# Performance work log

Hardware: AMD Instinct MI355X
Metric: run time of the kernel (lower is better)

Reference implementation:

```python
import jax, jax.numpy as jnp
import numpy as np

B, NUM, NVAR = 2048, 100, 11
NUM_OBS, NC = 10, 3
T_FIN = 10.0
RHO_OBS = 1.0; RHO_INEQ = 1.0; RHO_LANE = 1.0; RHO_PROJ = 1.0
W_SMOOTH = 20.0; W_VDES = 2.0; W_YDES = 1.0
A_EGO = 3.0; B_EGO = 1.5; MARGIN = 0.2
V_MIN = 0.001; V_MAX = 18.0; A_MAX = 6.0
MAXITER = 5
H = 256

def _basis():
    s = np.linspace(0.0, 1.0, NUM)
    j = np.arange(NVAR)
    P = s[:, None] ** j[None, :]
    Pd = np.zeros((NUM, NVAR)); Pdd = np.zeros((NUM, NVAR))
    Pd[:, 1:] = j[1:][None, :] * s[:, None] ** (j[1:] - 1)[None, :]
    Pdd[:, 2:] = (j[2:] * (j[2:] - 1))[None, :] * s[:, None] ** (j[2:] - 2)[None, :]
    return (jnp.asarray(P, jnp.float32), jnp.asarray(Pd / T_FIN, jnp.float32),
            jnp.asarray(Pdd / (T_FIN ** 2), jnp.float32))

P, PDOT, PDDOT = _basis()
A_EQ_X = jnp.stack([P[0], PDOT[0], PDDOT[0], P[-1]])   # [4, NVAR]
A_EQ_Y = jnp.stack([P[0], PDOT[0], PDDOT[0]])          # [3, NVAR]
PTP = P.T @ P

def _kkt_inv(Q, A):
    m = A.shape[0]
    K = jnp.concatenate([jnp.concatenate([Q, A.T], axis=1),
                         jnp.concatenate([A, jnp.zeros((m, m), jnp.float32)], axis=1)], axis=0)
    return jnp.linalg.inv(K)

# ADMM cost: rho_proj*I + smoothness + rho_obs*A_obs^T A_obs + rho_ineq*(Pdot^T Pdot + Pddot^T Pddot)
Q_COMMON = (RHO_PROJ + W_SMOOTH) * jnp.eye(NVAR, dtype=jnp.float32) \
    + RHO_OBS * NUM_OBS * NC * PTP \
    + RHO_INEQ * (PDOT.T @ PDOT + PDDOT.T @ PDDOT)
KKT_X = _kkt_inv(Q_COMMON, A_EQ_X)
KKT_Y = _kkt_inv(Q_COMMON + 2.0 * RHO_LANE * PTP, A_EQ_Y)   # A_lane = [P; -P]
# x_init QP (smoothness + v_des / y_des tracking)
Q_IX = W_SMOOTH * jnp.eye(NVAR, dtype=jnp.float32) + W_VDES * (PDOT.T @ PDOT)
KKT_IX = _kkt_inv(Q_IX, A_EQ_X)
KKT_IY = _kkt_inv(Q_IX + W_YDES * PTP, A_EQ_Y)


def _forward(init_state_ego, goal_des, closest_obs, psi_obs, dim_x_obs, dim_y_obs,
             y_ub, y_lb, gru_W_ih, gru_W_hh, gru_b, gru_h0,
             mlp_W1, mlp_b1, mlp_W2, mlp_b2):
    b = init_state_ego.shape[0]
    x0, y0, vx0, vy0, ax0, ay0 = (init_state_ego[:, i] for i in range(6))
    b_eq_x = jnp.stack([x0, vx0, ax0, goal_des[:, 0]], axis=1)   # [B,4]
    b_eq_y = jnp.stack([y0, vy0, ay0], axis=1)                    # [B,3]

    # ---- obstacle circle trajectories (static obstacles, vx=vy=0) ----
    xo = closest_obs[:, :NUM_OBS]; yo = closest_obs[:, NUM_OBS:2 * NUM_OBS]   # [B,O]
    r = jnp.stack([jnp.zeros_like(dim_x_obs),
                   (dim_x_obs - dim_y_obs) / 2,
                   -(dim_x_obs - dim_y_obs) / 2], axis=2)                      # [B,O,3]
    x_circ = xo[:, :, None] + r * jnp.cos(psi_obs)[:, :, None]                # [B,O,3]
    y_circ = yo[:, :, None] + r * jnp.sin(psi_obs)[:, :, None]
    shape4 = (b, NUM_OBS, NC, NUM)
    x_obs_f = jnp.broadcast_to(x_circ[..., None], shape4).reshape(b, -1)      # [B,O*C*T]
    y_obs_f = jnp.broadcast_to(y_circ[..., None], shape4).reshape(b, -1)
    rad = dim_y_obs / 2
    a_obs = jnp.broadcast_to((A_EGO + rad + MARGIN)[:, :, None, None], shape4).reshape(b, -1)
    b_obs = jnp.broadcast_to((B_EGO + rad + MARGIN)[:, :, None, None], shape4).reshape(b, -1)

    # ---- GRU context over obstacles -> learned lambda init ----
    feats = jnp.stack([xo, yo, dim_x_obs, dim_y_obs, psi_obs], axis=2)        # [B,O,5]
    def gru_step(h, x):
        gx = x @ gru_W_ih + gru_b
        gh = h @ gru_W_hh
        z = jax.nn.sigmoid(gx[:, :H] + gh[:, :H])
        rg = jax.nn.sigmoid(gx[:, H:2 * H] + gh[:, H:2 * H])
        n = jnp.tanh(gx[:, 2 * H:] + rg * gh[:, 2 * H:])
        return (1.0 - z) * n + z * h, None
    hT, _ = jax.lax.scan(gru_step, jnp.broadcast_to(gru_h0, (b, H)), jnp.swapaxes(feats, 0, 1))
    lam = jax.nn.relu(hT @ mlp_W1 + mlp_b1) @ mlp_W2 + mlp_b2                 # [B,2*NVAR]
    lam_x, lam_y = lam[:, :NVAR], lam[:, NVAR:]

    # ---- x_init: equality-constrained smoothness/tracking QP ----
    v_des = jnp.sqrt(vx0 ** 2 + vy0 ** 2)
    lin_ix = W_VDES * v_des[:, None] * jnp.sum(PDOT, axis=0)[None, :]
    lin_iy = W_YDES * goal_des[:, 1:2] * jnp.sum(P, axis=0)[None, :]
    c_x0 = (jnp.concatenate([lin_ix, b_eq_x], 1) @ KKT_IX.T)[:, :NVAR]
    c_y0 = (jnp.concatenate([lin_iy, b_eq_y], 1) @ KKT_IY.T)[:, :NVAR]

    b_lane = jnp.concatenate([y_ub[:, None] * jnp.ones((1, NUM), jnp.float32),
                              -y_lb[:, None] * jnp.ones((1, NUM), jnp.float32)], axis=1)  # [B,2T]

    def AobsT(v):   # A_obs^T v, v: [B, O*C*T] -> [B, NVAR]
        return v.reshape(b, NUM_OBS * NC, NUM).sum(axis=1) @ P

    def step(carry, _):
        c_x, c_y, lx, ly = carry
        x = c_x @ P.T; xd = c_x @ PDOT.T; xdd = c_x @ PDDOT.T
        y = c_y @ P.T; yd = c_y @ PDOT.T; ydd = c_y @ PDDOT.T
        wc = jnp.tile(x, (1, NUM_OBS * NC)) - x_obs_f
        ws = jnp.tile(y, (1, NUM_OBS * NC)) - y_obs_f
        alpha_o = jnp.arctan2(ws * a_obs, wc * b_obs)
        ca, sa = jnp.cos(alpha_o), jnp.sin(alpha_o)
        c1 = RHO_OBS * (a_obs ** 2 * ca ** 2 + b_obs ** 2 * sa ** 2)
        c2 = RHO_OBS * (a_obs * wc * ca + b_obs * ws * sa)
        d_o = jnp.maximum(1.0, c2 / c1)
        alpha_v = jnp.clip(jnp.arctan2(yd, xd), -0.41, 0.41)
        cv, sv = jnp.cos(alpha_v), jnp.sin(alpha_v)
        d_v = jnp.clip(xd * cv + yd * sv, V_MIN, V_MAX)
        alpha_a = jnp.arctan2(ydd + 1e-4, xdd + 1e-4)
        caa, saa = jnp.cos(alpha_a), jnp.sin(alpha_a)
        d_a = jnp.clip(xdd * caa + ydd * saa, 0.0, A_MAX)
        # targets
        b_ox = x_obs_f + a_obs * d_o * ca; b_oy = y_obs_f + b_obs * d_o * sa
        b_vx = d_v * cv; b_vy = d_v * sv
        b_ax = d_a * caa; b_ay = d_a * saa
        b_lane_aug = jnp.minimum(jnp.concatenate([y, -y], 1), b_lane)  # slack-augmented
        top_x = lx + RHO_PROJ * c_x0 + RHO_OBS * AobsT(b_ox) + RHO_INEQ * (b_vx @ PDOT + b_ax @ PDDOT)
        top_y = ly + RHO_PROJ * c_y0 + RHO_OBS * AobsT(b_oy) + RHO_INEQ * (b_vy @ PDOT + b_ay @ PDDOT) \
            + RHO_LANE * ((b_lane_aug[:, :NUM] - b_lane_aug[:, NUM:]) @ P)
        c_xn = (jnp.concatenate([top_x, b_eq_x], 1) @ KKT_X.T)[:, :NVAR]
        c_yn = (jnp.concatenate([top_y, b_eq_y], 1) @ KKT_Y.T)[:, :NVAR]
        # residuals / Lagrange multiplier updates
        xn = c_xn @ P.T; yn = c_yn @ P.T
        res_ox = jnp.tile(xn, (1, NUM_OBS * NC)) - b_ox
        res_oy = jnp.tile(yn, (1, NUM_OBS * NC)) - b_oy
        lxn = lx - RHO_OBS * AobsT(res_ox) \
            - RHO_INEQ * ((c_xn @ PDOT.T - b_vx) @ PDOT + (c_xn @ PDDOT.T - b_ax) @ PDDOT)
        res_lane = jnp.concatenate([yn, -yn], 1) - b_lane_aug
        lyn = ly - RHO_OBS * AobsT(res_oy) \
            - RHO_INEQ * ((c_yn @ PDOT.T - b_vy) @ PDOT + (c_yn @ PDDOT.T - b_ay) @ PDDOT) \
            - RHO_LANE * ((res_lane[:, :NUM] - res_lane[:, NUM:]) @ P)
        return (c_xn, c_yn, lxn, lyn), None

    (c_x, c_y, lam_x, lam_y), _ = jax.lax.scan(step, (c_x0, c_y0, lam_x, lam_y),
                                               None, length=MAXITER)
    return jnp.concatenate([c_x, c_y], axis=1)   # [B, 2*NVAR]


def setup_inputs() -> dict:
    key = jax.random.key(0)
    ks = jax.random.split(key, 12)
    d = {
        'init_state_ego': jax.random.normal(ks[0], (B, 6), jnp.float32),
        'goal_des': jax.random.normal(ks[1], (B, 2), jnp.float32),
        'closest_obs': jax.random.normal(ks[2], (B, 2 * NUM_OBS), jnp.float32),
        'psi_obs': jax.random.normal(ks[3], (B, NUM_OBS), jnp.float32),
        'dim_x_obs': jax.random.uniform(ks[4], (B, NUM_OBS), jnp.float32),
        'dim_y_obs': jax.random.uniform(ks[5], (B, NUM_OBS), jnp.float32),
        'y_ub': jnp.ones((B,), jnp.float32),
        'y_lb': jnp.zeros((B,), jnp.float32),
        'gru_W_ih': jax.random.normal(ks[6], (5, 3 * H), jnp.float32) / np.sqrt(5.0),
        'gru_W_hh': jax.random.normal(ks[7], (H, 3 * H), jnp.float32) / np.sqrt(float(H)),
        'gru_b': jnp.zeros((3 * H,), jnp.float32),
        'gru_h0': jax.random.normal(ks[8], (H,), jnp.float32) * 0.1,
        'mlp_W1': jax.random.normal(ks[9], (H, 512), jnp.float32) / np.sqrt(float(H)),
        'mlp_b1': jnp.zeros((512,), jnp.float32),
        'mlp_W2': jax.random.normal(ks[10], (512, 2 * NVAR), jnp.float32) / np.sqrt(512.0),
        'mlp_b2': jnp.zeros((2 * NVAR,), jnp.float32),
    }
    return d


def reference(init_state_ego, goal_des, closest_obs, psi_obs, dim_x_obs, dim_y_obs,
              y_ub, y_lb, gru_W_ih, gru_W_hh, gru_b, gru_h0,
              mlp_W1, mlp_b1, mlp_W2, mlp_b2):
    return _forward(init_state_ego, goal_des, closest_obs, psi_obs, dim_x_obs, dim_y_obs,
                    y_ub, y_lb, gru_W_ih, gru_W_hh, gru_b, gru_h0,
                    mlp_W1, mlp_b1, mlp_W2, mlp_b2)
```

## Files before the change

kernel.cpp:

```cpp
#include <hip/hip_runtime.h>
#include <math.h>

typedef short bf16x8 __attribute__((ext_vector_type(8)));
typedef float f32x4 __attribute__((ext_vector_type(4)));

__device__ __forceinline__ unsigned short f2bf(float x) {
  union { float f; unsigned u; } v; v.f = x;
  unsigned r = v.u + 0x7FFFu + ((v.u >> 16) & 1u);
  return (unsigned short)(r >> 16);
}
__device__ __forceinline__ float bf2f(unsigned short h) {
  union { unsigned u; float f; } v; v.u = ((unsigned)h) << 16; return v.f;
}

#define WS_WAUG  0u
#define WS_W1T   442368u
#define WS_HAUGA 704512u
#define WS_HAUGB 1884160u
#define WS_HF32  3063808u
#define WS_ACTS  3063808u
#define WS_LAM   5160960u
#define WS_KKT   5341184u
#define WS_GX    5344000u
#define WS_GY    5344704u
#define WS_MX    5345408u
#define WS_MY    5346112u
#define WS_SUMS  5346816u

__global__ __launch_bounds__(256) void prep(
    const float* __restrict__ Whh, const float* __restrict__ Wih,
    const float* __restrict__ gb, const float* __restrict__ W1,
    const float* __restrict__ h0,
    const float* __restrict__ obs, const float* __restrict__ dimx,
    const float* __restrict__ dimy, const float* __restrict__ psi,
    unsigned short* __restrict__ Waug, unsigned short* __restrict__ W1T,
    unsigned short* __restrict__ HaugA, unsigned short* __restrict__ HaugB,
    float* __restrict__ kkt_out, float* __restrict__ Gx_out,
    float* __restrict__ Gy_out, float* __restrict__ Mx_out,
    float* __restrict__ My_out, float* __restrict__ sums_out)
{
  __shared__ double S[21];
  __shared__ double aug[15][32];
  __shared__ double fbuf[15];
  __shared__ double Md[11][11];
  if (blockIdx.x < 4) {
    const int mat = blockIdx.x;
    const int n = (mat == 0 || mat == 2) ? 15 : 14;
    const int twoN = 2 * n;
    if (threadIdx.x == 0) {
      for (int m = 0; m < 21; ++m) S[m] = 0.0;
      for (int s = 0; s < 100; ++s) {
        double t = s * (1.0 / 99.0);
        double p = 1.0;
        for (int m = 0; m < 21; ++m) { S[m] += p; p *= t; }
      }
    }
    __syncthreads();
    for (int idx = threadIdx.x; idx < n * twoN; idx += 256) {
      int r = idx / twoN, c = idx % twoN;
      double v;
      if (c >= n) v = (c - n == r) ? 1.0 : 0.0;
      else if (r < 11 && c < 11) {
        double ptp = S[r + c];
        double pdp = (r >= 1 && c >= 1) ? ((double)(r * c) / 100.0) * S[r + c - 2] : 0.0;
        double pddp = (r >= 2 && c >= 2) ? ((double)(r*(r-1)) * (double)(c*(c-1)) / 10000.0) * S[r + c - 4] : 0.0;
        double dg = (r == c) ? 1.0 : 0.0;
        if (mat == 0)      v = 21.0*dg + 30.0*ptp + pdp + pddp;
        else if (mat == 1) v = 21.0*dg + 32.0*ptp + pdp + pddp;
        else if (mat == 2) v = 20.0*dg + 2.0*pdp;
        else               v = 20.0*dg + 2.0*pdp + ptp;
      } else if (r >= 11 && c >= 11) v = 0.0;
      else {
        int ar = (r >= 11) ? (r - 11) : (c - 11);
        int ac = (r >= 11) ? c : r;
        v = (ar == 0) ? ((ac == 0) ? 1.0 : 0.0)
          : (ar == 1) ? ((ac == 1) ? 0.1 : 0.0)
          : (ar == 2) ? ((ac == 2) ? 0.02 : 0.0)
          : 1.0;
      }
      aug[r][c] = v;
    }
    __syncthreads();
    for (int p = 0; p < n; ++p) {
      double pv = aug[p][p];
      __syncthreads();
      double inv = 1.0 / pv;
      for (int c = threadIdx.x; c < twoN; c += 256) aug[p][c] *= inv;
      __syncthreads();
      if (threadIdx.x < n) fbuf[threadIdx.x] = aug[threadIdx.x][p];
      __syncthreads();
      for (int idx = threadIdx.x; idx < n * twoN; idx += 256) {
        int r = idx / twoN, c = idx % twoN;
        if (r != p) aug[r][c] -= fbuf[r] * aug[p][c];
      }
      __syncthreads();
    }
    for (int idx = threadIdx.x; idx < 11 * n; idx += 256) {
      int r = idx / n, c = idx % n;
      kkt_out[mat * 176 + r * 16 + c] = (float)aug[r][n + c];
    }
    if (mat < 2) {
      if (threadIdx.x < 121) {
        int j = threadIdx.x / 11, i = threadIdx.x % 11;
        double m = 30.0 * S[j + i];
        if (j >= 1 && i >= 1) m += ((double)(j * i) / 100.0) * S[j + i - 2];
        if (j >= 2 && i >= 2) m += ((double)(j*(j-1)) * (double)(i*(i-1)) / 10000.0) * S[j + i - 4];
        if (mat == 1) m += 2.0 * S[j + i];
        Md[j][i] = m;
      }
      __syncthreads();
      if (threadIdx.x < 121) {
        int j = threadIdx.x / 11, i = threadIdx.x % 11;
        double g = (j == i) ? 1.0 : 0.0;
        for (int k = 0; k < 11; ++k) g -= Md[j][k] * aug[k][n + i];
        if (mat == 0) { Gx_out[j * 16 + i] = (float)g; Mx_out[j * 16 + i] = (float)Md[j][i]; }
        else          { Gy_out[j * 16 + i] = (float)g; My_out[j * 16 + i] = (float)Md[j][i]; }
      }
    }
    if (mat == 0 && threadIdx.x < 11) {
      int j = threadIdx.x;
      sums_out[j] = (float)S[j];
      sums_out[11 + j] = (j >= 1) ? (float)((double)j / 10.0 * S[j - 1]) : 0.f;
    }
    return;
  }
  int idx = (blockIdx.x - 4) * 256 + threadIdx.x;
  if (idx < 221184) {
    int col = idx / 288, k = idx - col * 288;
    float v;
    if (k < 256)       v = Whh[k * 768 + col];
    else if (k < 261)  v = Wih[(k - 256) * 768 + col];
    else if (k == 261) v = gb[col];
    else               v = 0.f;
    Waug[idx] = f2bf(v);
  } else if (idx < 352256) {
    int j = idx - 221184;
    int col = j >> 8, k = j & 255;
    W1T[j] = f2bf(W1[k * 512 + col]);
  } else if (idx < 942080) {
    int j = idx - 352256;
    int row = j / 288, k = j - row * 288;
    float v;
    if (k < 256)       v = h0[k];
    else if (k == 256) v = obs[row * 20 + 0];
    else if (k == 257) v = obs[row * 20 + 10];
    else if (k == 258) v = dimx[row * 10 + 0];
    else if (k == 259) v = dimy[row * 10 + 0];
    else if (k == 260) v = psi[row * 10 + 0];
    else if (k == 261) v = 1.0f;
    else               v = 0.f;
    HaugA[row * 288 + k] = f2bf(v);
  } else if (idx < 995328) {
    int j = idx - 942080;
    int row = j / 26, k = 262 + (j - row * 26);
    HaugB[row * 288 + k] = 0;
  }
}

#define MFMA __builtin_amdgcn_mfma_f32_16x16x32_bf16
__global__ __launch_bounds__(256) void gru_step(
    const unsigned short* __restrict__ Waug,
    const unsigned short* __restrict__ HaugC, unsigned short* __restrict__ HaugN,
    float* __restrict__ Hf32, const float* __restrict__ h0,
    const float* __restrict__ obs, const float* __restrict__ dimx,
    const float* __restrict__ dimy, const float* __restrict__ psi,
    int s)
{
  const int tid = threadIdx.x;
  const int m0 = blockIdx.x * 32;
  const int c0 = blockIdx.y * 32;
  const int lane = tid & 63, w = tid >> 6;
  const int l15 = lane & 15, g4 = lane >> 4;
  const int mi = w >> 1, cg = w & 1;

  const unsigned short* Arow = HaugC + (size_t)(m0 + mi * 16 + l15) * 288 + g4 * 8;
  const unsigned short* Bcol = Waug + (size_t)(c0 + cg * 16 + l15) * 288 + g4 * 8;

  f32x4 accz = {0.f,0.f,0.f,0.f}, accr = {0.f,0.f,0.f,0.f};
  f32x4 anh = {0.f,0.f,0.f,0.f}, anx = {0.f,0.f,0.f,0.f};

  #pragma unroll
  for (int kc = 0; kc < 9; ++kc) {
    bf16x8 a  = *(const bf16x8*)(Arow + kc * 32);
    bf16x8 bz = *(const bf16x8*)(Bcol + kc * 32);
    bf16x8 br = *(const bf16x8*)(Bcol + 256 * 288 + kc * 32);
    bf16x8 bn = *(const bf16x8*)(Bcol + 512 * 288 + kc * 32);
    accz = MFMA(a, bz, accz, 0, 0, 0);
    accr = MFMA(a, br, accr, 0, 0, 0);
    if (kc < 8) anh = MFMA(a, bn, anh, 0, 0, 0);
    else        anx = MFMA(a, bn, anx, 0, 0, 0);
  }

  const int colh = c0 + cg * 16 + l15;
  float h0c = (s == 0) ? h0[colh] : 0.f;
  #pragma unroll
  for (int rg = 0; rg < 4; ++rg) {
    int row = m0 + mi * 16 + g4 * 4 + rg;
    float hold = (s == 0) ? h0c : Hf32[(size_t)row * 256 + colh];
    float z = 1.f / (1.f + __expf(-accz[rg]));
    float rr = 1.f / (1.f + __expf(-accr[rg]));
    float nn = tanhf(anx[rg] + rr * anh[rg]);
    float hnew = (1.f - z) * nn + z * hold;
    Hf32[(size_t)row * 256 + colh] = hnew;
    HaugN[(size_t)row * 288 + colh] = f2bf(hnew);
  }
  if (blockIdx.y == 0 && s < 9 && tid < 192) {
    int row = m0 + tid / 6, e = tid - (tid / 6) * 6;
    int s1 = s + 1;
    float v = (e == 0) ? obs[row * 20 + s1] : (e == 1) ? obs[row * 20 + 10 + s1]
            : (e == 2) ? dimx[row * 10 + s1] : (e == 3) ? dimy[row * 10 + s1]
            : (e == 4) ? psi[row * 10 + s1] : 1.0f;
    HaugN[(size_t)row * 288 + 256 + e] = f2bf(v);
  }
}

__global__ __launch_bounds__(256) void mlp1(
    const unsigned short* __restrict__ Haug, const unsigned short* __restrict__ W1T,
    const float* __restrict__ b1, unsigned short* __restrict__ acts)
{
  __shared__ __align__(16) unsigned short As[8192];
  const int tid = threadIdx.x;
  const int m0 = blockIdx.x * 32, c0 = blockIdx.y * 128;
  const int lane = tid & 63, w = tid >> 6, l15 = lane & 15, g4 = lane >> 4;

  #pragma unroll
  for (int r = 0; r < 4; ++r) {
    int j = tid + 256 * r;
    int tile = j >> 6, q = j & 63, ci = q >> 2, ks = q & 3;
    int mi = tile >> 3, kc = tile & 7;
    const unsigned short* src = Haug + (size_t)(m0 + mi * 16 + ci) * 288 + kc * 32 + ks * 8;
    *(int4*)&As[tile * 512 + q * 8] = *(const int4*)src;
  }
  __syncthreads();

  const int foff = (l15 * 4 + g4) * 8;
  f32x4 acc[2][2];
  #pragma unroll
  for (int a = 0; a < 2; ++a)
    #pragma unroll
    for (int b = 0; b < 2; ++b) acc[a][b] = (f32x4){0.f,0.f,0.f,0.f};

  #pragma unroll
  for (int kc = 0; kc < 8; ++kc) {
    bf16x8 a0 = *(const bf16x8*)&As[(0 * 8 + kc) * 512 + foff];
    bf16x8 a1 = *(const bf16x8*)&As[(1 * 8 + kc) * 512 + foff];
    int kk = kc * 32 + g4 * 8;
    #pragma unroll
    for (int nt = 0; nt < 2; ++nt) {
      int col = c0 + w * 32 + nt * 16 + l15;
      bf16x8 b = *(const bf16x8*)&W1T[(size_t)col * 256 + kk];
      acc[0][nt] = MFMA(a0, b, acc[0][nt], 0, 0, 0);
      acc[1][nt] = MFMA(a1, b, acc[1][nt], 0, 0, 0);
    }
  }
  #pragma unroll
  for (int mi = 0; mi < 2; ++mi)
    #pragma unroll
    for (int nt = 0; nt < 2; ++nt) {
      int col = c0 + w * 32 + nt * 16 + l15;
      float bb = b1[col];
      #pragma unroll
      for (int rg = 0; rg < 4; ++rg) {
        int row = m0 + mi * 16 + g4 * 4 + rg;
        float v = fmaxf(acc[mi][nt][rg] + bb, 0.f);
        acts[(size_t)row * 512 + col] = f2bf(v);
      }
    }
}

__global__ __launch_bounds__(256) void mlp2(
    const unsigned short* __restrict__ acts, const float* __restrict__ W2,
    const float* __restrict__ b2, float* __restrict__ lam)
{
  __shared__ unsigned short Ablk[8 * 520];
  __shared__ float W2s[512 * 22];
  const int tid = threadIdx.x;
  const int m0 = blockIdx.x * 8;
  for (int i = tid; i < 4096; i += 256) {
    int r = i >> 9, k = i & 511;
    Ablk[r * 520 + k] = acts[(size_t)(m0 + r) * 512 + k];
  }
  for (int i = tid; i < 11264; i += 256) W2s[i] = W2[i];
  __syncthreads();
  if (tid < 176) {
    int row = tid / 22, col = tid - (tid / 22) * 22;
    float s = b2[col];
    const unsigned short* ap = &Ablk[row * 520];
    for (int k = 0; k < 512; ++k) s += bf2f(ap[k]) * W2s[k * 22 + col];
    lam[(size_t)(m0 + row) * 22 + col] = s;
  }
}

__global__ __launch_bounds__(128) void solver(
    const float* __restrict__ ise, const float* __restrict__ goal,
    const float* __restrict__ obs, const float* __restrict__ psi,
    const float* __restrict__ dimx, const float* __restrict__ dimy,
    const float* __restrict__ yub, const float* __restrict__ ylb,
    const float* __restrict__ lam, const float* __restrict__ kkt,
    const float* __restrict__ Gxm, const float* __restrict__ Gym,
    const float* __restrict__ Mxm, const float* __restrict__ Mym,
    const float* __restrict__ sums, float* __restrict__ out)
{
  __shared__ __align__(16) float Pt[3][11][108];
  __shared__ __align__(16) float red[7][108];
  __shared__ float redout[7][11];
  __shared__ float cx[11], cy[11], lx[11], ly[11], cx0[11], cy0[11];
  __shared__ float kxB[11], kyB[11], hx[11], hy[11];
  __shared__ float rhsx[15], rhsy[14];
  __shared__ float xc[30], yc[30], sa_[10], sb_[10], sab[10], sab2[10];

  const int b = blockIdx.x;
  const int tid = threadIdx.x;

  if (tid < 100) {
    float t = tid * (1.0f / 99.0f);
    float tjm2 = 0.f, tjm1 = 0.f, tj = 1.f;
    #pragma unroll
    for (int j = 0; j < 11; ++j) {
      Pt[0][j][tid] = tj;
      Pt[1][j][tid] = 0.1f * (float)j * tjm1;
      Pt[2][j][tid] = 0.01f * (float)(j * (j - 1)) * tjm2;
      tjm2 = tjm1; tjm1 = tj; tj *= t;
    }
  }
  if (tid < 10) {
    int o = tid;
    float xo = obs[b * 20 + o], yo = obs[b * 20 + 10 + o];
    float dx = dimx[b * 10 + o], dy = dimy[b * 10 + o], ps = psi[b * 10 + o];
    float sp, cp;
    __sincosf(ps, &sp, &cp);
    float r1 = 0.5f * (dx - dy);
    xc[o * 3] = xo; xc[o * 3 + 1] = xo + r1 * cp; xc[o * 3 + 2] = xo - r1 * cp;
    yc[o * 3] = yo; yc[o * 3 + 1] = yo + r1 * sp; yc[o * 3 + 2] = yo - r1 * sp;
    float rad = 0.5f * dy;
    float av = 3.2f + rad, bv = 1.7f + rad;
    sa_[o] = av; sb_[o] = bv; sab[o] = av * bv; sab2[o] = av * bv * av * bv;
  }
  if (tid < 11) { lx[tid] = lam[b * 22 + tid]; ly[tid] = lam[b * 22 + 11 + tid]; }
  const float vx0 = ise[b * 6 + 2], vy0 = ise[b * 6 + 3];
  if (tid == 0) {
    float x0 = ise[b * 6 + 0], y0 = ise[b * 6 + 1];
    float ax0 = ise[b * 6 + 4], ay0 = ise[b * 6 + 5];
    rhsx[11] = x0; rhsx[12] = vx0; rhsx[13] = ax0; rhsx[14] = goal[b * 2 + 0];
    rhsy[11] = y0; rhsy[12] = vy0; rhsy[13] = ay0;
  }
  {
    float vdes = sqrtf(vx0 * vx0 + vy0 * vy0);
    float gy = goal[b * 2 + 1];
    if (tid < 11) { rhsx[tid] = 2.f * vdes * sums[11 + tid]; rhsy[tid] = gy * sums[tid]; }
  }
  const float yU = yub[b], yL = ylb[b];
  __syncthreads();
  if (tid < 11) {
    const float* K = kkt + 2 * 176 + tid * 16;
    float s = 0.f;
    #pragma unroll
    for (int j = 0; j < 15; ++j) s += K[j] * rhsx[j];
    cx0[tid] = s; cx[tid] = s;
    const float* Kx = kkt + tid * 16;
    float kb = 0.f;
    #pragma unroll
    for (int c = 0; c < 4; ++c) kb += Kx[11 + c] * rhsx[11 + c];
    kxB[tid] = kb;
  } else if (tid >= 16 && tid < 27) {
    int i = tid - 16;
    const float* K = kkt + 3 * 176 + i * 16;
    float s = 0.f;
    #pragma unroll
    for (int j = 0; j < 14; ++j) s += K[j] * rhsy[j];
    cy0[i] = s; cy[i] = s;
    const float* Ky = kkt + 176 + i * 16;
    float kb = 0.f;
    #pragma unroll
    for (int c = 0; c < 3; ++c) kb += Ky[11 + c] * rhsy[11 + c];
    kyB[i] = kb;
  }
  __syncthreads();
  if (tid < 11) {
    float s = cx0[tid];
    #pragma unroll
    for (int i = 0; i < 11; ++i) s += Mxm[tid * 16 + i] * kxB[i];
    hx[tid] = s;
  } else if (tid >= 16 && tid < 27) {
    int j = tid - 16;
    float s = cy0[j];
    #pragma unroll
    for (int i = 0; i < 11; ++i) s += Mym[j * 16 + i] * kyB[i];
    hy[j] = s;
  }
  __syncthreads();

  for (int it = 0; it < 5; ++it) {
    if (tid < 100) {
      float t = tid * (1.0f / 99.0f);
      float x = 0, y = 0, xd = 0, yd = 0, xdd = 0, ydd = 0;
      {
        float tjm2 = 0, tjm1 = 0, tj = 1;
        #pragma unroll
        for (int j = 0; j < 11; ++j) {
          float cj = cx[j], dj = cy[j];
          x += cj * tj; y += dj * tj;
          float pd = 0.1f * (float)j * tjm1;
          xd += cj * pd; yd += dj * pd;
          float pdd = 0.01f * (float)(j * (j - 1)) * tjm2;
          xdd += cj * pdd; ydd += dj * pdd;
          tjm2 = tjm1; tjm1 = tj; tj *= t;
        }
      }
      float Sbx = 0.f, Sby = 0.f;
      for (int oi = 0; oi < 10; ++oi) {
        float A = sa_[oi], B = sb_[oi], AB = sab[oi], AB2 = sab2[oi];
        #pragma unroll
        for (int cc = 0; cc < 3; ++cc) {
          int o = oi * 3 + cc;
          float xcc = xc[o], ycc = yc[o];
          float wc = x - xcc, wsv = y - ycc;
          float p = wsv * A, q = wc * B;
          float h2 = p * p + q * q;
          float rin = rsqrtf(h2 + 1e-20f);
          float sc = AB * rin;
          bool outside = h2 >= AB2;
          Sbx += outside ? x : fmaf(wc, sc, xcc);
          Sby += outside ? y : fmaf(wsv, sc, ycc);
        }
      }
      bool clipv = (xd <= 0.f) || (fabsf(yd) > xd * 0.43463135f);
      float cv, sv;
      if (clipv) { cv = 0.91712081f; sv = copysignf(0.39860934f, yd); }
      else { float ri = rsqrtf(fmaxf(xd * xd + yd * yd, 1e-24f)); cv = xd * ri; sv = yd * ri; }
      float dv = fminf(fmaxf(xd * cv + yd * sv, 0.001f), 18.f);
      float qa = xdd + 1e-4f, pa = ydd + 1e-4f;
      float ria = rsqrtf(pa * pa + qa * qa + 1e-30f);
      float caa = qa * ria, saa = pa * ria;
      float da = fminf(fmaxf(xdd * caa + ydd * saa, 0.f), 6.f);
      red[0][tid] = Sbx; red[1][tid] = Sby;
      red[2][tid] = dv * cv; red[3][tid] = dv * sv;
      red[4][tid] = da * caa; red[5][tid] = da * saa;
      red[6][tid] = fminf(y, yU) - fminf(-y, -yL);
    }
    __syncthreads();
    if (tid < 77) {
      int a = tid / 11, j = tid - a * 11;
      int wt = (a < 2) ? 0 : (a < 4) ? 1 : (a < 6) ? 2 : 0;
      const float4* rp = (const float4*)(&red[a][0]);
      const float4* wp = (const float4*)(&Pt[wt][j][0]);
      float s = 0.f;
      #pragma unroll
      for (int k = 0; k < 25; ++k) {
        float4 rv = rp[k], wv = wp[k];
        s += rv.x * wv.x + rv.y * wv.y + rv.z * wv.z + rv.w * wv.w;
      }
      redout[a][j] = s;
    }
    __syncthreads();
    if (tid < 11) rhsx[tid] = lx[tid] + cx0[tid] + redout[0][tid] + redout[2][tid] + redout[4][tid];
    else if (tid >= 16 && tid < 27) {
      int j = tid - 16;
      rhsy[j] = ly[j] + cy0[j] + redout[1][j] + redout[3][j] + redout[5][j] + redout[6][j];
    }
    __syncthreads();
    if (tid < 11) {
      const float* K = kkt + tid * 16;
      const float* G = Gxm + tid * 16;
      float sc = kxB[tid], sl = -hx[tid];
      #pragma unroll
      for (int i = 0; i < 11; ++i) {
        float r = rhsx[i];
        sc += K[i] * r;
        sl += G[i] * r;
      }
      cx[tid] = sc; lx[tid] = sl;
    } else if (tid >= 16 && tid < 27) {
      int j = tid - 16;
      const float* K = kkt + 176 + j * 16;
      const float* G = Gym + j * 16;
      float sc = kyB[j], sl = -hy[j];
      #pragma unroll
      for (int i = 0; i < 11; ++i) {
        float r = rhsy[i];
        sc += K[i] * r;
        sl += G[i] * r;
      }
      cy[j] = sc; ly[j] = sl;
    }
    __syncthreads();
  }
  if (tid < 11) out[b * 22 + tid] = cx[tid];
  else if (tid >= 16 && tid < 27) out[b * 22 + 11 + (tid - 16)] = cy[tid - 16];
}

extern "C" void kernel_launch(void* const* d_in, const int* in_sizes, int n_in,
                              void* d_out, int out_size, void* d_ws, size_t ws_size,
                              hipStream_t stream) {
  const float* ise  = (const float*)d_in[0];
  const float* goal = (const float*)d_in[1];
  const float* obs  = (const float*)d_in[2];
  const float* psi  = (const float*)d_in[3];
  const float* dimx = (const float*)d_in[4];
  const float* dimy = (const float*)d_in[5];
  const float* yub  = (const float*)d_in[6];
  const float* ylb  = (const float*)d_in[7];
  const float* Wih  = (const float*)d_in[8];
  const float* Whh  = (const float*)d_in[9];
  const float* gb   = (const float*)d_in[10];
  const float* h0   = (const float*)d_in[11];
  const float* W1   = (const float*)d_in[12];
  const float* b1   = (const float*)d_in[13];
  const float* W2   = (const float*)d_in[14];
  const float* b2   = (const float*)d_in[15];

  char* ws = (char*)d_ws;
  unsigned short* Waug  = (unsigned short*)(ws + WS_WAUG);
  unsigned short* W1T   = (unsigned short*)(ws + WS_W1T);
  unsigned short* HaugA = (unsigned short*)(ws + WS_HAUGA);
  unsigned short* HaugB = (unsigned short*)(ws + WS_HAUGB);
  float* Hf32 = (float*)(ws + WS_HF32);
  unsigned short* acts = (unsigned short*)(ws + WS_ACTS);
  float* lamb = (float*)(ws + WS_LAM);
  float* kkt  = (float*)(ws + WS_KKT);
  float* Gxm  = (float*)(ws + WS_GX);
  float* Gym  = (float*)(ws + WS_GY);
  float* Mxm  = (float*)(ws + WS_MX);
  float* Mym  = (float*)(ws + WS_MY);
  float* sums = (float*)(ws + WS_SUMS);

  prep<<<3892, 256, 0, stream>>>(Whh, Wih, gb, W1, h0, obs, dimx, dimy, psi,
                                 Waug, W1T, HaugA, HaugB, kkt, Gxm, Gym, Mxm, Mym, sums);
  for (int s = 0; s < 10; ++s) {
    const unsigned short* hc = (s & 1) ? HaugB : HaugA;
    unsigned short* hn = (s & 1) ? HaugA : HaugB;
    gru_step<<<dim3(64, 8), 256, 0, stream>>>(Waug, hc, hn, Hf32, h0,
                                              obs, dimx, dimy, psi, s);
  }
  mlp1<<<dim3(64, 4), 256, 0, stream>>>(HaugA, W1T, b1, acts);
  mlp2<<<256, 256, 0, stream>>>(acts, W2, b2, lamb);
  solver<<<2048, 128, 0, stream>>>(ise, goal, obs, psi, dimx, dimy, yub, ylb,
                                   lamb, kkt, Gxm, Gym, Mxm, Mym, sums, (float*)d_out);
  (void)in_sizes; (void)n_in; (void)out_size; (void)ws_size;
}
```

Before: 245.3 us.

## Fuse MLP layers into one MFMA kernel and drop solver rhs sync

Measured after the change: 262.9 us. +7.2%, slower.

```diff
diff --git a/kernel.cpp b/kernel.cpp
--- a/kernel.cpp
+++ b/kernel.cpp
@@ -18,7 +18,6 @@
 #define WS_HAUGA 704512u
 #define WS_HAUGB 1884160u
 #define WS_HF32  3063808u
-#define WS_ACTS  3063808u
 #define WS_LAM   5160960u
 #define WS_KKT   5341184u
 #define WS_GX    5344000u
@@ -26,14 +25,16 @@
 #define WS_MX    5345408u
 #define WS_MY    5346112u
 #define WS_SUMS  5346816u
+#define WS_W2T   5346944u
 
 __global__ __launch_bounds__(256) void prep(
     const float* __restrict__ Whh, const float* __restrict__ Wih,
     const float* __restrict__ gb, const float* __restrict__ W1,
-    const float* __restrict__ h0,
+    const float* __restrict__ W2, const float* __restrict__ h0,
     const float* __restrict__ obs, const float* __restrict__ dimx,
     const float* __restrict__ dimy, const float* __restrict__ psi,
     unsigned short* __restrict__ Waug, unsigned short* __restrict__ W1T,
+    unsigned short* __restrict__ W2T,
     unsigned short* __restrict__ HaugA, unsigned short* __restrict__ HaugB,
     float* __restrict__ kkt_out, float* __restrict__ Gx_out,
     float* __restrict__ Gy_out, float* __restrict__ Mx_out,
@@ -154,6 +155,10 @@
     int j = idx - 942080;
     int row = j / 26, k = 262 + (j - row * 26);
     HaugB[row * 288 + k] = 0;
+  } else if (idx < 1011712) {
+    int j = idx - 995328;
+    int col = j >> 9, k = j & 511;
+    W2T[j] = f2bf(col < 22 ? W2[k * 22 + col] : 0.f);
   }
 }
 
@@ -214,80 +219,70 @@
   }
 }
 
-__global__ __launch_bounds__(256) void mlp1(
+__global__ __launch_bounds__(256) void mlp_fused(
     const unsigned short* __restrict__ Haug, const unsigned short* __restrict__ W1T,
-    const float* __restrict__ b1, unsigned short* __restrict__ acts)
+    const float* __restrict__ b1, const unsigned short* __restrict__ W2T,
+    const float* __restrict__ b2, float* __restrict__ lam)
 {
-  __shared__ __align__(16) unsigned short As[8192];
+  __shared__ __align__(16) unsigned short As[4096];
+  __shared__ __align__(16) unsigned short Acts[8192];
   const int tid = threadIdx.x;
-  const int m0 = blockIdx.x * 32, c0 = blockIdx.y * 128;
+  const int m0 = blockIdx.x * 16;
   const int lane = tid & 63, w = tid >> 6, l15 = lane & 15, g4 = lane >> 4;
 
   #pragma unroll
-  for (int r = 0; r < 4; ++r) {
+  for (int r = 0; r < 2; ++r) {
     int j = tid + 256 * r;
     int tile = j >> 6, q = j & 63, ci = q >> 2, ks = q & 3;
-    int mi = tile >> 3, kc = tile & 7;
-    const unsigned short* src = Haug + (size_t)(m0 + mi * 16 + ci) * 288 + kc * 32 + ks * 8;
+    const unsigned short* src = Haug + (size_t)(m0 + ci) * 288 + tile * 32 + ks * 8;
     *(int4*)&As[tile * 512 + q * 8] = *(const int4*)src;
   }
   __syncthreads();
-
   const int foff = (l15 * 4 + g4) * 8;
-  f32x4 acc[2][2];
+
+  f32x4 acc[8];
   #pragma unroll
-  for (int a = 0; a < 2; ++a)
-    #pragma unroll
-    for (int b = 0; b < 2; ++b) acc[a][b] = (f32x4){0.f,0.f,0.f,0.f};
-
+  for (int nt = 0; nt < 8; ++nt) acc[nt] = (f32x4){0.f,0.f,0.f,0.f};
   #pragma unroll
   for (int kc = 0; kc < 8; ++kc) {
-    bf16x8 a0 = *(const bf16x8*)&As[(0 * 8 + kc) * 512 + foff];
-    bf16x8 a1 = *(const bf16x8*)&As[(1 * 8 + kc) * 512 + foff];
+    bf16x8 a = *(const bf16x8*)&As[kc * 512 + foff];
     int kk = kc * 32 + g4 * 8;
     #pragma unroll
-    for (int nt = 0; nt < 2; ++nt) {
-      int col = c0 + w * 32 + nt * 16 + l15;
+    for (int nt = 0; nt < 8; ++nt) {
+      int col = w * 128 + nt * 16 + l15;
       bf16x8 b = *(const bf16x8*)&W1T[(size_t)col * 256 + kk];
-      acc[0][nt] = MFMA(a0, b, acc[0][nt], 0, 0, 0);
-      acc[1][nt] = MFMA(a1, b, acc[1][nt], 0, 0, 0);
+      acc[nt] = MFMA(a, b, acc[nt], 0, 0, 0);
     }
   }
   #pragma unroll
-  for (int mi = 0; mi < 2; ++mi)
-    #pragma unroll
-    for (int nt = 0; nt < 2; ++nt) {
-      int col = c0 + w * 32 + nt * 16 + l15;
-      float bb = b1[col];
+  for (int nt = 0; nt < 8; ++nt) {
+    int col = w * 128 + nt * 16 + l15;
+    float bb = b1[col];
+    int tile = col >> 5, sub = (col >> 3) & 3, e = col & 7;
+    #pragma unroll
+    for (int rg = 0; rg < 4; ++rg) {
+      int row = g4 * 4 + rg;
+      float v = fmaxf(acc[nt][rg] + bb, 0.f);
+      Acts[tile * 512 + (row * 4 + sub) * 8 + e] = f2bf(v);
+    }
+  }
+  __syncthreads();
+
+  if (w < 2) {
+    int col = w * 16 + l15;
+    f32x4 a2 = {0.f,0.f,0.f,0.f};
+    #pragma unroll
+    for (int kc = 0; kc < 16; ++kc) {
+      bf16x8 a = *(const bf16x8*)&Acts[kc * 512 + foff];
+      bf16x8 b = *(const bf16x8*)&W2T[(size_t)col * 512 + kc * 32 + g4 * 8];
+      a2 = MFMA(a, b, a2, 0, 0, 0);
+    }
+    if (col < 22) {
+      float bb = b2[col];
       #pragma unroll
-      for (int rg = 0; rg < 4; ++rg) {
-        int row = m0 + mi * 16 + g4 * 4 + rg;
-        float v = fmaxf(acc[mi][nt][rg] + bb, 0.f);
-        acts[(size_t)row * 512 + col] = f2bf(v);
-      }
-    }
-}
-
-__global__ __launch_bounds__(256) void mlp2(
-    const unsigned short* __restrict__ acts, const float* __restrict__ W2,
-    const float* __restrict__ b2, float* __restrict__ lam)
-{
-  __shared__ unsigned short Ablk[8 * 520];
-  __shared__ float W2s[512 * 22];
-  const int tid = threadIdx.x;
-  const int m0 = blockIdx.x * 8;
-  for (int i = tid; i < 4096; i += 256) {
-    int r = i >> 9, k = i & 511;
-    Ablk[r * 520 + k] = acts[(size_t)(m0 + r) * 512 + k];
-  }
-  for (int i = tid; i < 11264; i += 256) W2s[i] = W2[i];
-  __syncthreads();
-  if (tid < 176) {
-    int row = tid / 22, col = tid - (tid / 22) * 22;
-    float s = b2[col];
-    const unsigned short* ap = &Ablk[row * 520];
-    for (int k = 0; k < 512; ++k) s += bf2f(ap[k]) * W2s[k * 22 + col];
-    lam[(size_t)(m0 + row) * 22 + col] = s;
+      for (int rg = 0; rg < 4; ++rg)
+        lam[(size_t)(m0 + g4 * 4 + rg) * 22 + col] = a2[rg] + bb;
+    }
   }
 }
 
@@ -453,19 +448,13 @@
       redout[a][j] = s;
     }
     __syncthreads();
-    if (tid < 11) rhsx[tid] = lx[tid] + cx0[tid] + redout[0][tid] + redout[2][tid] + redout[4][tid];
-    else if (tid >= 16 && tid < 27) {
-      int j = tid - 16;
-      rhsy[j] = ly[j] + cy0[j] + redout[1][j] + redout[3][j] + redout[5][j] + redout[6][j];
-    }
-    __syncthreads();
     if (tid < 11) {
       const float* K = kkt + tid * 16;
       const float* G = Gxm + tid * 16;
       float sc = kxB[tid], sl = -hx[tid];
       #pragma unroll
       for (int i = 0; i < 11; ++i) {
-        float r = rhsx[i];
+        float r = lx[i] + cx0[i] + redout[0][i] + redout[2][i] + redout[4][i];
         sc += K[i] * r;
         sl += G[i] * r;
       }
@@ -477,7 +466,7 @@
       float sc = kyB[j], sl = -hy[j];
       #pragma unroll
       for (int i = 0; i < 11; ++i) {
-        float r = rhsy[i];
+        float r = ly[i] + cy0[i] + redout[1][i] + redout[3][i] + redout[5][i] + redout[6][i];
         sc += K[i] * r;
         sl += G[i] * r;
       }
@@ -512,10 +501,10 @@
   char* ws = (char*)d_ws;
   unsigned short* Waug  = (unsigned short*)(ws + WS_WAUG);
   unsigned short* W1T   = (unsigned short*)(ws + WS_W1T);
+  unsigned short* W2T   = (unsigned short*)(ws + WS_W2T);
   unsigned short* HaugA = (unsigned short*)(ws + WS_HAUGA);
   unsigned short* HaugB = (unsigned short*)(ws + WS_HAUGB);
   float* Hf32 = (float*)(ws + WS_HF32);
-  unsigned short* acts = (unsigned short*)(ws + WS_ACTS);
   float* lamb = (float*)(ws + WS_LAM);
   float* kkt  = (float*)(ws + WS_KKT);
   float* Gxm  = (float*)(ws + WS_GX);
@@ -524,16 +513,16 @@
   float* Mym  = (float*)(ws + WS_MY);
   float* sums = (float*)(ws + WS_SUMS);
 
-  prep<<<3892, 256, 0, stream>>>(Whh, Wih, gb, W1, h0, obs, dimx, dimy, psi,
-                                 Waug, W1T, HaugA, HaugB, kkt, Gxm, Gym, Mxm, Mym, sums);
+  prep<<<3956, 256, 0, stream>>>(Whh, Wih, gb, W1, W2, h0, obs, dimx, dimy, psi,
+                                 Waug, W1T, W2T, HaugA, HaugB,
+                                 kkt, Gxm, Gym, Mxm, Mym, sums);
   for (int s = 0; s < 10; ++s) {
     const unsigned short* hc = (s & 1) ? HaugB : HaugA;
     unsigned short* hn = (s & 1) ? HaugA : HaugB;
     gru_step<<<dim3(64, 8), 256, 0, stream>>>(Waug, hc, hn, Hf32, h0,
                                               obs, dimx, dimy, psi, s);
   }
-  mlp1<<<dim3(64, 4), 256, 0, stream>>>(HaugA, W1T, b1, acts);
-  mlp2<<<256, 256, 0, stream>>>(acts, W2, b2, lamb);
+  mlp_fused<<<128, 256, 0, stream>>>(HaugA, W1T, b1, W2T, b2, lamb);
   solver<<<2048, 128, 0, stream>>>(ise, goal, obs, psi, dimx, dimy, yub, ylb,
                                    lamb, kkt, Gxm, Gym, Mxm, Mym, sums, (float*)d_out);
   (void)in_sizes; (void)n_in; (void)out_size; (void)ws_size;
```
